# Performance work log

Measured on AMD Instinct MI355X. Metric: run time of the kernel, lower is better.

Reference implementation:

```python
import jax, jax.numpy as jnp
import numpy as np

GROUPS = 8
EPS = 1e-5


def setup_inputs() -> dict:
    key = jax.random.key(0)
    ks = jax.random.split(key, 3)
    b, c, h, w = 8, 256, 64, 64
    return {
        "x": jax.random.normal(ks[0], (b, c, h, w), dtype=jnp.float32),
        "norm_w": jnp.ones((c,), jnp.float32),
        "norm_b": jnp.zeros((c,), jnp.float32),
        "qkv_w": jax.random.normal(ks[1], (3 * c, c), dtype=jnp.float32) * (1.0 / np.sqrt(c)),
        "qkv_b": jnp.zeros((3 * c,), jnp.float32),
        "proj_w": jax.random.normal(ks[2], (c, c), dtype=jnp.float32) * (1.0 / np.sqrt(c)),
        "proj_b": jnp.zeros((c,), jnp.float32),
    }


def _group_norm(x, w, b):
    B, C, H, W = x.shape
    xg = x.reshape(B, GROUPS, C // GROUPS, H, W)
    mean = xg.mean(axis=(2, 3, 4), keepdims=True)
    var = xg.var(axis=(2, 3, 4), keepdims=True)
    xn = ((xg - mean) * jax.lax.rsqrt(var + EPS)).reshape(B, C, H, W)
    return xn * w[None, :, None, None] + b[None, :, None, None]


def reference(x, norm_w, norm_b, qkv_w, qkv_b, proj_w, proj_b):
    B, C, H, W = x.shape
    xn = _group_norm(x, norm_w, norm_b)
    # 1x1 conv == per-pixel matmul: [B,3C,H,W]
    qkv = jnp.einsum('bchw,oc->bohw', xn, qkv_w) + qkv_b[None, :, None, None]
    q, k, v = jnp.split(qkv, 3, axis=1)  # each [B,C,H,W]
    hw = H * W
    q = q.reshape(B, C, hw).transpose(0, 2, 1)  # [B,hw,C]
    k = k.reshape(B, C, hw)                     # [B,C,hw]
    v = v.reshape(B, C, hw).transpose(0, 2, 1)  # [B,hw,C]
    scores = jnp.einsum('bnc,bcm->bnm', q, k) / jnp.sqrt(jnp.asarray(C, x.dtype))
    attn = jax.nn.softmax(scores, axis=-1)      # [B,hw,hw]
    out = jnp.einsum('bnm,bmc->bnc', attn, v)   # [B,hw,C]
    out = out.transpose(0, 2, 1).reshape(B, C, H, W)
    out = jnp.einsum('bchw,oc->bohw', out, proj_w) + proj_b[None, :, None, None]
    return x + out
```

## Files before the change

kernel.cpp:

```cpp
#include <hip/hip_runtime.h>
#include <stdint.h>

#define BATCH 8
#define CH 256
#define HW 4096
#define OC 768

typedef __bf16 bf16;
typedef __attribute__((ext_vector_type(8))) __bf16 bf16x8;
typedef __attribute__((ext_vector_type(4))) __bf16 bf16x4;
typedef __attribute__((ext_vector_type(4))) float f32x4;
typedef long fp8x8;

#define MFMA16(a, b, c) __builtin_amdgcn_mfma_f32_16x16x32_bf16(a, b, c, 0, 0, 0)
#define MFMA8(a, b, c) __builtin_amdgcn_mfma_f32_16x16x32_fp8_fp8(a, b, c, 0, 0, 0)
#define LOG2E 1.44269504088896f

static __device__ __forceinline__ void gl2lds16(const void* g, void* l) {
  __builtin_amdgcn_global_load_lds((const __attribute__((address_space(1))) void*)g,
                                   (__attribute__((address_space(3))) void*)l, 16, 0, 0);
}

static __device__ __forceinline__ int pack4fp8(float a, float b, float c, float d) {
  int t = __builtin_amdgcn_cvt_pk_fp8_f32(a, b, 0, false);
  return __builtin_amdgcn_cvt_pk_fp8_f32(c, d, t, true);
}

__global__ __launch_bounds__(256) void trans_stats(const float* __restrict__ x,
    bf16* __restrict__ xt, float* __restrict__ partial) {
  __shared__ float tile[32][33];
  __shared__ float red[8];
  int b = blockIdx.z, ct = blockIdx.y, pt = blockIdx.x;
  int p0 = pt * 32, c0 = ct * 32;
  const float* xb = x + (size_t)b * CH * HW;
  float s = 0.f, s2 = 0.f;
#pragma unroll
  for (int i = 0; i < 4; i++) {
    int c = c0 + threadIdx.y + i * 8;
    float v = xb[(size_t)c * HW + p0 + threadIdx.x];
    tile[threadIdx.y + i * 8][threadIdx.x] = v;
    s += v;
    s2 += v * v;
  }
  int tid = threadIdx.y * 32 + threadIdx.x;
  for (int off = 32; off; off >>= 1) { s += __shfl_down(s, off); s2 += __shfl_down(s2, off); }
  if ((tid & 63) == 0) { red[(tid >> 6) * 2] = s; red[(tid >> 6) * 2 + 1] = s2; }
  __syncthreads();
  if (tid == 0) {
    float* pp = partial + ((size_t)(b * 8 + ct) * 128 + pt) * 2;
    pp[0] = red[0] + red[2] + red[4] + red[6];
    pp[1] = red[1] + red[3] + red[5] + red[7];
  }
  bf16* xtb = xt + (size_t)b * HW * CH;
#pragma unroll
  for (int i = 0; i < 4; i++) {
    int p = p0 + threadIdx.y + i * 8;
    xtb[(size_t)p * CH + c0 + threadIdx.x] = (bf16)tile[threadIdx.x][threadIdx.y + i * 8];
  }
}

__global__ __launch_bounds__(128) void gn_finalize(const float* __restrict__ partial,
    const float* __restrict__ nw, const float* __restrict__ nb,
    float* __restrict__ scale, float* __restrict__ shift) {
  int bg = blockIdx.x;
  int t = threadIdx.x;
  const float* pp = partial + (size_t)bg * 128 * 2;
  float s = pp[t * 2], s2 = pp[t * 2 + 1];
  __shared__ float red[4], mm[2];
  for (int off = 32; off; off >>= 1) { s += __shfl_down(s, off); s2 += __shfl_down(s2, off); }
  if ((t & 63) == 0) { red[(t >> 6) * 2] = s; red[(t >> 6) * 2 + 1] = s2; }
  __syncthreads();
  if (t == 0) {
    float ts = red[0] + red[2], ts2 = red[1] + red[3];
    float mean = ts * (1.0f / 131072.0f);
    float var = ts2 * (1.0f / 131072.0f) - mean * mean;
    mm[0] = mean;
    mm[1] = rsqrtf(var + 1e-5f);
  }
  __syncthreads();
  if (t < 32) {
    int b = bg >> 3, g = bg & 7, c = g * 32 + t;
    float sc = nw[c] * mm[1];
    scale[b * CH + c] = sc;
    shift[b * CH + c] = nb[c] - mm[0] * sc;
  }
}

__global__ __launch_bounds__(256) void fold_qkv(const float* __restrict__ qkv_w,
    const float* __restrict__ qkv_b, const float* __restrict__ scale,
    const float* __restrict__ shift, bf16* __restrict__ wq, float* __restrict__ bq) {
  int o = blockIdx.x, b = blockIdx.y, c = threadIdx.x;
  float w = qkv_w[o * CH + c];
  wq[((size_t)b * OC + o) * CH + c] = (bf16)(w * scale[b * CH + c]);
  float part = w * shift[b * CH + c];
  __shared__ float red[4];
  for (int off = 32; off; off >>= 1) part += __shfl_down(part, off);
  if ((threadIdx.x & 63) == 0) red[threadIdx.x >> 6] = part;
  __syncthreads();
  if (threadIdx.x == 0) bq[b * OC + o] = qkv_b[o] + red[0] + red[1] + red[2] + red[3];
}

__global__ __launch_bounds__(256) void conv_projw(const float* __restrict__ w,
                                                  bf16* __restrict__ wb) {
  int i = blockIdx.x * 256 + threadIdx.x;
  wb[i] = (bf16)w[i];
}

__global__ __launch_bounds__(256) void qkv_gemm(const bf16* __restrict__ wq,
    const float* __restrict__ bq, const bf16* __restrict__ xt,
    uint8_t* __restrict__ qt, uint8_t* __restrict__ kt, uint8_t* __restrict__ vv) {
  __shared__ __align__(16) bf16 As[2][128 * 32];
  __shared__ __align__(16) bf16 Bs[2][128 * 32];
  int b = blockIdx.z, row0 = blockIdx.y * 128, col0 = blockIdx.x * 128;
  const bf16* A = wq + (size_t)b * OC * CH + (size_t)row0 * CH;
  const bf16* Bt = xt + (size_t)b * HW * CH + (size_t)col0 * CH;
  int tid = threadIdx.x, lane = tid & 63, wave = tid >> 6;
  int wm = (wave & 1) * 64, wn = (wave >> 1) * 64;
  int l15 = lane & 15, quad = lane >> 4;
  auto stage = [&](int buf, int k0) {
#pragma unroll
    for (int i = 0; i < 2; i++) {
      int idx = i * 256 + tid, r = idx >> 2, ch = idx & 3;
      gl2lds16(A + (size_t)r * CH + k0 + ch * 8, &As[buf][idx * 8]);
    }
#pragma unroll
    for (int i = 0; i < 2; i++) {
      int idx = i * 256 + tid, r = idx >> 2, ch = idx & 3;
      gl2lds16(Bt + (size_t)r * CH + k0 + ch * 8, &Bs[buf][idx * 8]);
    }
  };
  f32x4 zero = {0.f, 0.f, 0.f, 0.f};
  f32x4 acc[4][4];
#pragma unroll
  for (int i = 0; i < 4; i++)
#pragma unroll
    for (int j = 0; j < 4; j++) acc[i][j] = zero;
  stage(0, 0);
  for (int kk = 0; kk < 8; kk++) {
    int cur = kk & 1;
    __syncthreads();
    if (kk < 7) stage(1 - cur, (kk + 1) * 32);
    bf16x8 af[4], bfr[4];
#pragma unroll
    for (int i = 0; i < 4; i++) {
      af[i] = *(const bf16x8*)(&As[cur][(wm + i * 16 + l15) * 32 + quad * 8]);
      bfr[i] = *(const bf16x8*)(&Bs[cur][(wn + i * 16 + l15) * 32 + quad * 8]);
    }
#pragma unroll
    for (int i = 0; i < 4; i++)
#pragma unroll
      for (int j = 0; j < 4; j++) acc[i][j] = MFMA16(af[i], bfr[j], acc[i][j]);
  }
#pragma unroll
  for (int i = 0; i < 4; i++) {
    int o = row0 + wm + i * 16 + quad * 4;
#pragma unroll
    for (int j = 0; j < 4; j++) {
      int p = col0 + wn + j * 16 + l15;
      float v[4];
#pragma unroll
      for (int r = 0; r < 4; r++) v[r] = acc[i][j][r] + bq[b * OC + o + r];
      if (o < CH) {
        *(int*)(qt + ((size_t)b * HW + p) * CH + o) =
            pack4fp8(v[0] * LOG2E, v[1] * LOG2E, v[2] * LOG2E, v[3] * LOG2E);
      } else if (o < 2 * CH) {
        *(int*)(kt + ((size_t)b * HW + p) * CH + (o - CH)) = pack4fp8(v[0], v[1], v[2], v[3]);
      } else {
#pragma unroll
        for (int r = 0; r < 4; r++) {
          int t8 = __builtin_amdgcn_cvt_pk_fp8_f32(v[r], 0.f, 0, false);
          vv[((size_t)b * CH + (o - 2 * CH + r)) * HW + p] = (uint8_t)(t8 & 0xff);
        }
      }
    }
  }
}

__global__ __launch_bounds__(256, 2) void attn(const uint8_t* __restrict__ qt,
    const uint8_t* __restrict__ kt, const uint8_t* __restrict__ vv,
    bf16* __restrict__ opart, float* __restrict__ lstat) {
  __shared__ __align__(16) uint8_t Ks[2][32 * 256];
  __shared__ __align__(16) uint8_t Vs[3][256 * 32];
  int b = blockIdx.z, mh = blockIdx.y, q0 = blockIdx.x * 128;
  int tid = threadIdx.x, lane = tid & 63, w = tid >> 6;
  int l15 = lane & 15, quad = lane >> 4;
  int q1 = quad >> 1, qh = quad & 1;
  const uint8_t* kb_base = kt + (size_t)b * HW * CH;
  const uint8_t* vb_base = vv + (size_t)b * CH * HW;
  auto stageK = [&](int buf, int m0) {
    const uint8_t* kb = kb_base + (size_t)m0 * CH;
#pragma unroll
    for (int i = 0; i < 2; i++) {
      int idx = i * 256 + tid, m = idx >> 4, p16 = idx & 15;
      gl2lds16(kb + m * CH + (p16 ^ (m & 7)) * 16, &Ks[buf][idx * 16]);
    }
  };
  auto stageV = [&](int buf, int m0) {
#pragma unroll
    for (int i = 0; i < 2; i++) {
      int idx = i * 256 + tid, c = idx >> 1;
      int h2 = (idx & 1) ^ ((idx >> 3) & 1);
      gl2lds16(vb_base + (size_t)c * HW + m0 + h2 * 16, &Vs[buf][idx * 16]);
    }
  };
  fp8x8 qf[2][8];
  const uint8_t* qb = qt + ((size_t)b * HW + q0 + w * 32) * CH;
#pragma unroll
  for (int ns = 0; ns < 2; ns++)
#pragma unroll
    for (int kc = 0; kc < 8; kc++)
      qf[ns][kc] = *(const fp8x8*)(qb + (size_t)(ns * 16 + l15) * CH + kc * 32 + quad * 8);
  f32x4 zero = {0.f, 0.f, 0.f, 0.f};
  f32x4 o[2][16];
#pragma unroll
  for (int ns = 0; ns < 2; ns++)
#pragma unroll
    for (int t = 0; t < 16; t++) o[ns][t] = zero;
  float lsum[2] = {0.f, 0.f};
  int kswz = l15 & 7;
  int vswz = (l15 >> 2) & 1;
  fp8x8 pa[2];

  auto qk = [&](int kbuf, f32x4 (&s)[2][2]) {
#pragma unroll
    for (int kc = 0; kc < 8; kc++) {
      fp8x8 kf[2];
#pragma unroll
      for (int ms = 0; ms < 2; ms++)
        kf[ms] = *(const fp8x8*)(&Ks[kbuf][(ms * 16 + l15) * 256 +
                                           (((kc * 2 + q1) ^ kswz) * 16) + qh * 8]);
#pragma unroll
      for (int ms = 0; ms < 2; ms++)
#pragma unroll
        for (int ns = 0; ns < 2; ns++) s[ms][ns] = MFMA8(kf[ms], qf[ns][kc], s[ms][ns]);
    }
  };
  auto softmax = [&](f32x4 (&s)[2][2]) {
#pragma unroll
    for (int ns = 0; ns < 2; ns++) {
      float p0[4], p1[4];
#pragma unroll
      for (int r = 0; r < 4; r++) {
        p0[r] = exp2f(fmaf(s[0][ns][r], 0.0625f, -2.0f));
        lsum[ns] += p0[r];
      }
#pragma unroll
      for (int r = 0; r < 4; r++) {
        p1[r] = exp2f(fmaf(s[1][ns][r], 0.0625f, -2.0f));
        lsum[ns] += p1[r];
      }
      int pk0 = pack4fp8(p0[0], p0[1], p0[2], p0[3]);
      int pk1 = pack4fp8(p1[0], p1[1], p1[2], p1[3]);
      int srcLo = ((quad & 1) * 32 + l15) << 2;
      int srcHi = srcLo + 64;
      int a0 = __builtin_amdgcn_ds_bpermute(srcLo, pk0);
      int a1 = __builtin_amdgcn_ds_bpermute(srcLo, pk1);
      int b0 = __builtin_amdgcn_ds_bpermute(srcHi, pk0);
      int b1 = __builtin_amdgcn_ds_bpermute(srcHi, pk1);
      int2 pr;
      pr.x = q1 ? a1 : a0;
      pr.y = q1 ? b1 : b0;
      pa[ns] = __builtin_bit_cast(long, pr);
    }
  };
  auto pv = [&](int vbuf) {
#pragma unroll
    for (int t = 0; t < 16; t++) {
      fp8x8 vf = *(const fp8x8*)(&Vs[vbuf][(2 * (t * 16 + l15) + (q1 ^ vswz)) * 16 + qh * 8]);
      o[0][t] = MFMA8(vf, pa[0], o[0][t]);
      o[1][t] = MFMA8(vf, pa[1], o[1][t]);
    }
  };

  int m0base = mh * 2048;
  stageK(0, m0base);
  stageV(0, m0base);
  stageK(1, m0base + 32);
  stageV(1, m0base + 32);
  __syncthreads();
  {
    f32x4 s[2][2] = {{zero, zero}, {zero, zero}};
    qk(0, s);
    softmax(s);
  }
  int vread = 0;
  int vstage = 2;
  for (int i = 1; i < 64; i++) {
    int kcur = i & 1;
    __syncthreads();
    if (i < 63) {
      int m0n = m0base + (i + 1) * 32;
      stageK(1 - kcur, m0n);
      stageV(vstage, m0n);
      vstage = (vstage == 2) ? 0 : vstage + 1;
    }
    f32x4 s[2][2] = {{zero, zero}, {zero, zero}};
    __builtin_amdgcn_s_setprio(1);
    qk(kcur, s);
    pv(vread);
    __builtin_amdgcn_s_setprio(0);
    softmax(s);
    vread = (vread == 2) ? 0 : vread + 1;
  }
  pv(vread);
  int ncol = q0 + w * 32 + l15;
#pragma unroll
  for (int ns = 0; ns < 2; ns++) {
    float lt = lsum[ns];
    lt += __shfl_xor(lt, 16);
    lt += __shfl_xor(lt, 32);
    float inv = 1.0f / lt;
    bf16* ob = opart + (size_t)(mh * BATCH + b) * CH * HW + ncol + ns * 16;
#pragma unroll
    for (int t = 0; t < 16; t++)
#pragma unroll
      for (int r = 0; r < 4; r++)
        ob[(size_t)(t * 16 + quad * 4 + r) * HW] = (bf16)(o[ns][t][r] * inv);
    if (quad == 0)
      lstat[(size_t)(mh * BATCH + b) * HW + ncol + ns * 16] = lt;
  }
}

__global__ __launch_bounds__(256) void combine_t(const bf16* __restrict__ opart,
    const float* __restrict__ lstat, bf16* __restrict__ ot) {
  __shared__ float tile[32][33];
  int b = blockIdx.z, p0 = blockIdx.x * 32, c0 = blockIdx.y * 32;
  int tx = threadIdx.x, ty = threadIdx.y;
  int p = p0 + tx;
  float l0 = lstat[(size_t)(0 * BATCH + b) * HW + p];
  float l1 = lstat[(size_t)(1 * BATCH + b) * HW + p];
  float inv = 1.0f / (l0 + l1);
  float w0 = l0 * inv, w1 = l1 * inv;
#pragma unroll
  for (int i = 0; i < 4; i++) {
    int c = c0 + ty + i * 8;
    tile[ty + i * 8][tx] =
        w0 * (float)opart[((size_t)(0 * BATCH + b) * CH + c) * HW + p] +
        w1 * (float)opart[((size_t)(1 * BATCH + b) * CH + c) * HW + p];
  }
  __syncthreads();
#pragma unroll
  for (int i = 0; i < 4; i++) {
    int pp = p0 + ty + i * 8;
    ot[((size_t)b * HW + pp) * CH + c0 + tx] = (bf16)tile[tx][ty + i * 8];
  }
}

__global__ __launch_bounds__(256) void proj_gemm(const bf16* __restrict__ pw,
    const float* __restrict__ pbias, const bf16* __restrict__ ot,
    const float* __restrict__ x, float* __restrict__ out) {
  __shared__ __align__(16) bf16 As[2][128 * 32];
  __shared__ __align__(16) bf16 Bs[2][128 * 32];
  int b = blockIdx.z, row0 = blockIdx.y * 128, col0 = blockIdx.x * 128;
  const bf16* A = pw + (size_t)row0 * CH;
  const bf16* Bt = ot + (size_t)b * HW * CH + (size_t)col0 * CH;
  int tid = threadIdx.x, lane = tid & 63, wave = tid >> 6;
  int wm = (wave & 1) * 64, wn = (wave >> 1) * 64;
  int l15 = lane & 15, quad = lane >> 4;
  auto stage = [&](int buf, int k0) {
#pragma unroll
    for (int i = 0; i < 2; i++) {
      int idx = i * 256 + tid, r = idx >> 2, ch = idx & 3;
      gl2lds16(A + (size_t)r * CH + k0 + ch * 8, &As[buf][idx * 8]);
    }
#pragma unroll
    for (int i = 0; i < 2; i++) {
      int idx = i * 256 + tid, r = idx >> 2, ch = idx & 3;
      gl2lds16(Bt + (size_t)r * CH + k0 + ch * 8, &Bs[buf][idx * 8]);
    }
  };
  f32x4 zero = {0.f, 0.f, 0.f, 0.f};
  f32x4 acc[4][4];
#pragma unroll
  for (int i = 0; i < 4; i++)
#pragma unroll
    for (int j = 0; j < 4; j++) acc[i][j] = zero;
  stage(0, 0);
  for (int kk = 0; kk < 8; kk++) {
    int cur = kk & 1;
    __syncthreads();
    if (kk < 7) stage(1 - cur, (kk + 1) * 32);
    bf16x8 af[4], bfr[4];
#pragma unroll
    for (int i = 0; i < 4; i++) {
      af[i] = *(const bf16x8*)(&As[cur][(wm + i * 16 + l15) * 32 + quad * 8]);
      bfr[i] = *(const bf16x8*)(&Bs[cur][(wn + i * 16 + l15) * 32 + quad * 8]);
    }
#pragma unroll
    for (int i = 0; i < 4; i++)
#pragma unroll
      for (int j = 0; j < 4; j++) acc[i][j] = MFMA16(af[i], bfr[j], acc[i][j]);
  }
#pragma unroll
  for (int i = 0; i < 4; i++) {
#pragma unroll
    for (int j = 0; j < 4; j++) {
      int p = col0 + wn + j * 16 + l15;
#pragma unroll
      for (int r = 0; r < 4; r++) {
        int oo = row0 + wm + i * 16 + quad * 4 + r;
        size_t off = ((size_t)b * CH + oo) * HW + p;
        out[off] = x[off] + pbias[oo] + acc[i][j][r];
      }
    }
  }
}

extern "C" void kernel_launch(void* const* d_in, const int* in_sizes, int n_in,
                              void* d_out, int out_size, void* d_ws, size_t ws_size,
                              hipStream_t stream) {
  const float* x = (const float*)d_in[0];
  const float* nw = (const float*)d_in[1];
  const float* nb = (const float*)d_in[2];
  const float* qkvw = (const float*)d_in[3];
  const float* qkvb = (const float*)d_in[4];
  const float* projw = (const float*)d_in[5];
  const float* projb = (const float*)d_in[6];
  float* out = (float*)d_out;
  char* ws = (char*)d_ws;
  float* scale = (float*)(ws + 0);
  float* shift = (float*)(ws + 8192);
  float* bq    = (float*)(ws + 16384);
  bf16* pwb    = (bf16*)(ws + 40960);
  bf16* wq     = (bf16*)(ws + 172032);
  bf16* xt     = (bf16*)(ws + 3317760);
  uint8_t* qt  = (uint8_t*)(ws + 20094976);
  uint8_t* kt  = (uint8_t*)(ws + 36872192);
  uint8_t* vv  = (uint8_t*)(ws + 53649408);
  bf16* opart  = (bf16*)(ws + 70426624);
  float* lstat = (float*)(ws + 103981056);
  float* partial = (float*)(ws + 70426624);
  bf16* ot = xt;

  trans_stats<<<dim3(128, 8, 8), dim3(32, 8), 0, stream>>>(x, xt, partial);
  gn_finalize<<<64, 128, 0, stream>>>(partial, nw, nb, scale, shift);
  fold_qkv<<<dim3(768, 8), 256, 0, stream>>>(qkvw, qkvb, scale, shift, wq, bq);
  conv_projw<<<256, 256, 0, stream>>>(projw, pwb);
  qkv_gemm<<<dim3(32, 6, 8), 256, 0, stream>>>(wq, bq, xt, qt, kt, vv);
  attn<<<dim3(32, 2, 8), 256, 0, stream>>>(qt, kt, vv, opart, lstat);
  combine_t<<<dim3(128, 8, 8), dim3(32, 8), 0, stream>>>(opart, lstat, ot);
  proj_gemm<<<dim3(32, 2, 8), 256, 0, stream>>>(pwb, projb, ot, x, out);
}
```

Measured before the change: 292.6 us.

## Interleave softmax between PV halves and remap block indices for L2 locality

The loop is restructured so softmax of the current tile runs between two halves of the PV MFMA chain from the previous tile. Double-buffered P registers (paA/paB) and a 2x-unrolled loop make this possible, and the priority window now covers the softmax too. The aim is to hide exp and permute latency behind matrix work. Separately, the block index is linearised and remapped so that concurrently scheduled blocks span batch and key-half pairs differently, which changes cache locality. The extra live P registers may add register pressure under the 2-waves launch bound.

```diff
diff --git a/kernel.cpp b/kernel.cpp
--- a/kernel.cpp
+++ b/kernel.cpp
@@ -181,7 +181,9 @@
     bf16* __restrict__ opart, float* __restrict__ lstat) {
   __shared__ __align__(16) uint8_t Ks[2][32 * 256];
   __shared__ __align__(16) uint8_t Vs[3][256 * 32];
-  int b = blockIdx.z, mh = blockIdx.y, q0 = blockIdx.x * 128;
+  int lin = blockIdx.x + 32 * (blockIdx.y + 2 * blockIdx.z);
+  int pair = (lin & 7) * 2 + ((lin >> 3) & 1);
+  int b = pair >> 1, mh = pair & 1, q0 = (lin >> 4) * 128;
   int tid = threadIdx.x, lane = tid & 63, w = tid >> 6;
   int l15 = lane & 15, quad = lane >> 4;
   int q1 = quad >> 1, qh = quad & 1;
@@ -219,7 +221,6 @@
   float lsum[2] = {0.f, 0.f};
   int kswz = l15 & 7;
   int vswz = (l15 >> 2) & 1;
-  fp8x8 pa[2];
 
   auto qk = [&](int kbuf, f32x4 (&s)[2][2]) {
 #pragma unroll
@@ -235,7 +236,7 @@
         for (int ns = 0; ns < 2; ns++) s[ms][ns] = MFMA8(kf[ms], qf[ns][kc], s[ms][ns]);
     }
   };
-  auto softmax = [&](f32x4 (&s)[2][2]) {
+  auto softmax = [&](f32x4 (&s)[2][2], fp8x8 (&paOut)[2]) {
 #pragma unroll
     for (int ns = 0; ns < 2; ns++) {
       float p0[4], p1[4];
@@ -260,12 +261,13 @@
       int2 pr;
       pr.x = q1 ? a1 : a0;
       pr.y = q1 ? b1 : b0;
-      pa[ns] = __builtin_bit_cast(long, pr);
-    }
-  };
-  auto pv = [&](int vbuf) {
-#pragma unroll
-    for (int t = 0; t < 16; t++) {
+      paOut[ns] = __builtin_bit_cast(long, pr);
+    }
+  };
+  auto pv_half = [&](int vbuf, fp8x8 (&pa)[2], int t0) {
+#pragma unroll
+    for (int t8 = 0; t8 < 8; t8++) {
+      int t = t0 + t8;
       fp8x8 vf = *(const fp8x8*)(&Vs[vbuf][(2 * (t * 16 + l15) + (q1 ^ vswz)) * 16 + qh * 8]);
       o[0][t] = MFMA8(vf, pa[0], o[0][t]);
       o[1][t] = MFMA8(vf, pa[1], o[1][t]);
@@ -273,19 +275,20 @@
   };
 
   int m0base = mh * 2048;
+  int vread = 0;
+  int vstage = 2;
   stageK(0, m0base);
   stageV(0, m0base);
   stageK(1, m0base + 32);
   stageV(1, m0base + 32);
   __syncthreads();
+  fp8x8 paA[2], paB[2];
   {
     f32x4 s[2][2] = {{zero, zero}, {zero, zero}};
     qk(0, s);
-    softmax(s);
-  }
-  int vread = 0;
-  int vstage = 2;
-  for (int i = 1; i < 64; i++) {
+    softmax(s, paA);
+  }
+  auto body = [&](int i, fp8x8 (&paPrev)[2], fp8x8 (&paCur)[2]) {
     int kcur = i & 1;
     __syncthreads();
     if (i < 63) {
@@ -297,12 +300,19 @@
     f32x4 s[2][2] = {{zero, zero}, {zero, zero}};
     __builtin_amdgcn_s_setprio(1);
     qk(kcur, s);
-    pv(vread);
+    pv_half(vread, paPrev, 0);
+    softmax(s, paCur);
+    pv_half(vread, paPrev, 8);
     __builtin_amdgcn_s_setprio(0);
-    softmax(s);
     vread = (vread == 2) ? 0 : vread + 1;
-  }
-  pv(vread);
+  };
+  for (int ii = 1; ii <= 61; ii += 2) {
+    body(ii, paA, paB);
+    body(ii + 1, paB, paA);
+  }
+  body(63, paA, paB);
+  pv_half(vread, paB, 0);
+  pv_half(vread, paB, 8);
   int ncol = q0 + w * 32 + l15;
 #pragma unroll
   for (int ns = 0; ns < 2; ns++) {
```

After: 292.3 us. Within noise of the previous version (-0.1%).
